# Performance work log

Hardware: AMD Instinct MI355X
Metric: run time of the kernel (lower is better)

Reference implementation:

```python
import jax, jax.numpy as jnp
import numpy as np

HIDDEN = 1024
HEADS = 16
HEAD_DIM = HIDDEN // HEADS


def setup_inputs() -> dict:
    key = jax.random.key(0)
    k0, k1, k2, k3, k4 = jax.random.split(key, 5)
    s = 0.02
    return {
        "data": jax.random.normal(k0, (4, 2048, HIDDEN), dtype=jnp.float32),
        "qkv_w": jax.random.normal(k1, (3 * HIDDEN, HIDDEN), dtype=jnp.float32) * s,  # (out,in) torch layout
        "qkv_b": jax.random.normal(k2, (3 * HIDDEN,), dtype=jnp.float32) * s,
        "out_w": jax.random.normal(k3, (HIDDEN, HIDDEN), dtype=jnp.float32) * s,
        "out_b": jax.random.normal(k4, (HIDDEN,), dtype=jnp.float32) * s,
    }


def reference(data, qkv_w, qkv_b, out_w, out_b):
    B, T, C = data.shape
    qkv = jnp.einsum("btc,oc->bto", data, qkv_w) + qkv_b  # [B,T,3C]
    q, k, v = jnp.split(qkv, 3, axis=2)
    # [B,T,C] -> [B,H,T,D]
    def heads(x):
        return x.reshape(B, T, HEADS, HEAD_DIM).transpose(0, 2, 1, 3)
    q, k, v = heads(q), heads(k), heads(v)
    scale = 1.0 / jnp.sqrt(jnp.float32(HEAD_DIM))
    att = jnp.einsum("bhqd,bhkd->bhqk", q, k) * scale  # [B,H,T,T]
    causal = jnp.tril(jnp.ones((T, T), dtype=bool))
    att = jnp.where(causal[None, None, :, :], att, -jnp.inf)
    att = jax.nn.softmax(att, axis=-1)
    out = jnp.einsum("bhqk,bhkd->bhqd", att, v)  # [B,H,T,D]
    out = out.transpose(0, 2, 1, 3).reshape(B, T, C)
    return jnp.einsum("btc,oc->bto", out, out_w) + out_b
```

## Files before the change

### kernel.cpp

```cpp
#include <hip/hip_runtime.h>
#include <hip/hip_bf16.h>
#include <stdint.h>

typedef __attribute__((ext_vector_type(8))) __bf16 bf16x8;
typedef __attribute__((ext_vector_type(4))) float f32x4;
typedef __attribute__((ext_vector_type(16))) float f32x16;
typedef __attribute__((ext_vector_type(4))) unsigned int u32x4;

#define HIDDEN 1024
#define HEADS 16
#define HD 64
#define NB 4
#define T_ 2048
#define M_ROWS (NB * T_)
#define SCL2 0.18033688f
#define FIXM 32.0f

__device__ __forceinline__ unsigned short f2bf(float x) {
  unsigned u = __builtin_bit_cast(unsigned, x);
  u += 0x7fff + ((u >> 16) & 1);
  return (unsigned short)(u >> 16);
}

__device__ __forceinline__ unsigned pk2(float a, float b) {
  unsigned ua = __builtin_bit_cast(unsigned, a) + 0x8000u;
  unsigned ub = __builtin_bit_cast(unsigned, b) + 0x8000u;
  return __builtin_amdgcn_perm(ub, ua, 0x07060302);
}

__device__ __forceinline__ f32x4 mfma16(bf16x8 a, bf16x8 b, f32x4 c) {
  return __builtin_amdgcn_mfma_f32_16x16x32_bf16(a, b, c, 0, 0, 0);
}
__device__ __forceinline__ f32x16 mfma32(bf16x8 a, bf16x8 b, f32x16 c) {
  return __builtin_amdgcn_mfma_f32_32x32x16_bf16(a, b, c, 0, 0, 0);
}

__device__ __forceinline__ void lds16(const void* g, void* l) {
  __builtin_amdgcn_global_load_lds(
      (const __attribute__((address_space(1))) unsigned int*)g,
      (__attribute__((address_space(3))) unsigned int*)l, 16, 0, 0);
}

__device__ __forceinline__ bf16x8 ldg8(const unsigned short* p) {
  return __builtin_bit_cast(bf16x8, *(const u32x4*)p);
}

__global__ void cvt_bf16(const float* __restrict__ in,
                         unsigned short* __restrict__ out, int n4) {
  int i = blockIdx.x * blockDim.x + threadIdx.x;
  int stride = gridDim.x * blockDim.x;
  for (; i < n4; i += stride) {
    float4 v = ((const float4*)in)[i];
    ushort4 o;
    o.x = f2bf(v.x); o.y = f2bf(v.y); o.z = f2bf(v.z); o.w = f2bf(v.w);
    ((ushort4*)out)[i] = o;
  }
}


#define MF4(AM, B0, B1, B2, B3, M)              \
  acc[M][0] = mfma16(AM, B0, acc[M][0]);        \
  acc[M][1] = mfma16(AM, B1, acc[M][1]);        \
  acc[M][2] = mfma16(AM, B2, acc[M][2]);        \
  acc[M][3] = mfma16(AM, B3, acc[M][3]);

#define RD(BUF, OFF) \
  __builtin_bit_cast(bf16x8, *(const u32x4*)((BUF) + (OFF)))

template <int EPI, int NT>
__global__ __launch_bounds__(512, 2) void gemm8(
    const unsigned short* __restrict__ A, const unsigned short* __restrict__ Bm,
    const float* __restrict__ bias, unsigned short* __restrict__ Qb,
    unsigned short* __restrict__ Kb, unsigned short* __restrict__ Vtb,
    float* __restrict__ Cf) {
  constexpr int K = 1024;
  constexpr int N = NT * 128;
  __shared__ __align__(16) char LB[147456];
  const int tid = threadIdx.x;
  const int wv = tid >> 6, lane = tid & 63;
  const int l16 = lane & 15, grp = lane >> 4;
  const int wm = wv >> 1, wn = wv & 1;
  const int bid = blockIdx.x;
  const int sw = (bid & 7) * (NT * 4) + (bid >> 3);
  const int by = sw / NT, bx = sw % NT;
  const int brow0 = by * 256, bcol0 = bx * 128;

  const int srow = wv * 8 + (lane >> 3);
  const int sunit = (lane & 7) ^ (srow & 7);
  const unsigned short* pA = A + (size_t)(brow0 + srow) * K + sunit * 8;
  const unsigned short* pB = Bm + (size_t)(bcol0 + srow) * K + sunit * 8;

  const int rsw = l16 & 7;
  const int swu0 = ((grp) ^ rsw) << 4;
  const int swu1 = ((4 + grp) ^ rsw) << 4;
  const int aBase = (wm * 64 + l16) * 128;
  const int bBase = (wn * 64 + l16) * 128;

#define BUFA(c) (LB + (c) * 49152)
#define BUFB(c) (LB + (c) * 49152 + 32768)
#define STAGE_A01(c, t)                                          \
  do {                                                           \
    lds16(pA + (size_t)(t) * 64, BUFA(c) + wv * 1024);           \
    lds16(pA + (size_t)64 * K + (t) * 64,                        \
          BUFA(c) + 8192 + wv * 1024);                           \
  } while (0)
#define STAGE_A23(c, t)                                          \
  do {                                                           \
    lds16(pA + (size_t)128 * K + (t) * 64,                       \
          BUFA(c) + 16384 + wv * 1024);                          \
    lds16(pA + (size_t)192 * K + (t) * 64,                       \
          BUFA(c) + 24576 + wv * 1024);                          \
  } while (0)
#define STAGE_B01(c, t)                                          \
  do {                                                           \
    lds16(pB + (size_t)(t) * 64, BUFB(c) + wv * 1024);           \
    lds16(pB + (size_t)64 * K + (t) * 64,                        \
          BUFB(c) + 8192 + wv * 1024);                           \
  } while (0)

  f32x4 acc[4][4];
#pragma unroll
  for (int m = 0; m < 4; m++)
#pragma unroll
    for (int n = 0; n < 4; n++) acc[m][n] = (f32x4){0.f, 0.f, 0.f, 0.f};

#define GTILE(BA, BB, S1, S2, S3, ENDW)                                \
  {                                                                    \
    bf16x8 b00 = RD(BB, bBase + swu0), b01 = RD(BB, bBase + 2048 + swu0), \
           b02 = RD(BB, bBase + 4096 + swu0),                          \
           b03 = RD(BB, bBase + 6144 + swu0);                          \
    bf16x8 a0 = RD(BA, aBase + swu0), a1 = RD(BA, aBase + 2048 + swu0); \
    S1;                                                                \
    __builtin_amdgcn_s_barrier();                                      \
    __builtin_amdgcn_s_setprio(1);                                     \
    MF4(a0, b00, b01, b02, b03, 0)                                     \
    MF4(a1, b00, b01, b02, b03, 1)                                     \
    __builtin_amdgcn_s_setprio(0);                                     \
    __builtin_amdgcn_s_barrier();                                      \
    bf16x8 b10 = RD(BB, bBase + swu1), b11 = RD(BB, bBase + 2048 + swu1), \
           b12 = RD(BB, bBase + 4096 + swu1),                          \
           b13 = RD(BB, bBase + 6144 + swu1);                          \
    a0 = RD(BA, aBase + swu1);                                         \
    a1 = RD(BA, aBase + 2048 + swu1);                                  \
    S2;                                                                \
    __builtin_amdgcn_s_barrier();                                      \
    __builtin_amdgcn_s_setprio(1);                                     \
    MF4(a0, b10, b11, b12, b13, 0)                                     \
    MF4(a1, b10, b11, b12, b13, 1)                                     \
    __builtin_amdgcn_s_setprio(0);                                     \
    __builtin_amdgcn_s_barrier();                                      \
    a0 = RD(BA, aBase + 4096 + swu0);                                  \
    a1 = RD(BA, aBase + 6144 + swu0);                                  \
    S3;                                                                \
    __builtin_amdgcn_s_barrier();                                      \
    __builtin_amdgcn_s_setprio(1);                                     \
    MF4(a0, b00, b01, b02, b03, 2)                                     \
    MF4(a1, b00, b01, b02, b03, 3)                                     \
    __builtin_amdgcn_s_setprio(0);                                     \
    __builtin_amdgcn_s_barrier();                                      \
    a0 = RD(BA, aBase + 4096 + swu1);                                  \
    a1 = RD(BA, aBase + 6144 + swu1);                                  \
    __builtin_amdgcn_s_barrier();                                      \
    __builtin_amdgcn_s_setprio(1);                                     \
    MF4(a0, b10, b11, b12, b13, 2)                                     \
    MF4(a1, b10, b11, b12, b13, 3)                                     \
    __builtin_amdgcn_s_setprio(0);                                     \
    ENDW;                                                              \
    __builtin_amdgcn_s_barrier();                                      \
  }

  STAGE_A01(0, 0); STAGE_A23(0, 0); STAGE_B01(0, 0);
  STAGE_A01(1, 1); STAGE_A23(1, 1); STAGE_B01(1, 1);
  asm volatile("s_waitcnt vmcnt(6)" ::: "memory");
  __builtin_amdgcn_sched_barrier(0);
  __builtin_amdgcn_s_barrier();

  int c = 0, c2 = 2;
#pragma unroll 1
  for (int t = 0; t < 14; ++t) {
    const char* ba = BUFA(c);
    const char* bb = BUFB(c);
    GTILE(ba, bb, STAGE_A01(c2, t + 2), STAGE_A23(c2, t + 2),
          STAGE_B01(c2, t + 2),
          { asm volatile("s_waitcnt vmcnt(6)" ::: "memory");
            __builtin_amdgcn_sched_barrier(0); });
    c = (c == 2) ? 0 : c + 1;
    c2 = (c2 == 2) ? 0 : c2 + 1;
  }
  {
    const char* ba = BUFA(c);
    const char* bb = BUFB(c);
    GTILE(ba, bb, , , ,
          { asm volatile("s_waitcnt vmcnt(0)" ::: "memory");
            __builtin_amdgcn_sched_barrier(0); });
    c = (c == 2) ? 0 : c + 1;
  }
  {
    const char* ba = BUFA(c);
    const char* bb = BUFB(c);
    GTILE(ba, bb, , , , );
  }

#pragma unroll
  for (int m = 0; m < 4; m++) {
#pragma unroll
    for (int n = 0; n < 4; n++) {
      int col = bcol0 + wn * 64 + n * 16 + l16;
      int row0 = brow0 + wm * 64 + m * 16 + grp * 4;
      float bs = bias[col];
      if (EPI == 0) {
        int part = col >> 10, rem = col & 1023;
        int h = rem >> 6, d = rem & 63;
#pragma unroll
        for (int r = 0; r < 4; r++) {
          int rw = row0 + r;
          int b = rw >> 11, t = rw & 2047;
          unsigned short val = f2bf(acc[m][n][r] + bs);
          size_t bh = (size_t)(b * 16 + h);
          if (part == 0)
            Qb[(bh * T_ + t) * HD + d] = val;
          else if (part == 1)
            Kb[(bh * T_ + t) * HD + d] = val;
          else {
            int k = t & 31;
            int rr = (k & 3) + 4 * (k >> 3);
            int s = (rr & 7) + 8 * ((k >> 2) & 1) + 16 * (rr >> 3);
            Vtb[(bh * HD + d) * T_ + (t & ~31) + s] = val;
          }
        }
      } else {
#pragma unroll
        for (int r = 0; r < 4; r++)
          Cf[(size_t)(row0 + r) * N + col] = acc[m][n][r] + bs;
      }
    }
  }
#undef BUFA
#undef BUFB
#undef STAGE_A01
#undef STAGE_A23
#undef STAGE_B01
#undef GTILE
}

__global__ __launch_bounds__(256, 3) void attn32(
    const unsigned short* __restrict__ Q, const unsigned short* __restrict__ K,
    const unsigned short* __restrict__ Vt, unsigned short* __restrict__ Ao) {
  __shared__ __align__(16) unsigned short Kl[2][32 * 64];
  __shared__ __align__(16) unsigned short Vl[2][32 * 64];
  const int i = blockIdx.x;
  const int bh = i & 63;
  const int g = (i < 512) ? (15 - (i >> 6)) : ((i - 512) >> 6);
  const int wv = threadIdx.x >> 6, lane = threadIdx.x & 63;
  const int l31 = lane & 31, hi = lane >> 5;
  const int qt = g * 4 + wv;
  const int maxqt = g * 4 + 3;
  const unsigned short* Qh = Q + (size_t)bh * T_ * HD;
  const unsigned short* Kh = K + (size_t)bh * T_ * HD;
  const unsigned short* Vh = Vt + (size_t)bh * HD * T_;
  const int b_ = bh >> 4, h_ = bh & 15;

  const int sj = threadIdx.x >> 3, su = threadIdx.x & 7;
  const int sup = su ^ (sj & 7);
  const unsigned short* ksrc = Kh + sj * HD + sup * 8;
  const unsigned short* vsrc =
      Vh + (size_t)(sj + 32 * (sup >> 2)) * T_ + (sup & 3) * 8;
  char* kdst0 = (char*)&Kl[0][0] + wv * 1024;
  char* kdst1 = (char*)&Kl[1][0] + wv * 1024;
  char* vdst0 = (char*)&Vl[0][0] + wv * 1024;
  char* vdst1 = (char*)&Vl[1][0] + wv * 1024;

#define STAGE(B, KC)                                     \
  do {                                                   \
    int kt_ = (KC) * 32;                                 \
    lds16(ksrc + (size_t)kt_ * HD, (B) ? kdst1 : kdst0); \
    lds16(vsrc + kt_, (B) ? vdst1 : vdst0);              \
  } while (0)

  int rdoff[4];
#pragma unroll
  for (int ks = 0; ks < 4; ks++)
    rdoff[ks] = l31 * 128 + (((2 * ks + hi) ^ (l31 & 7)) << 4);

  bf16x8 qf[4];
  const int qbase = qt * 32;
#pragma unroll
  for (int st = 0; st < 4; st++)
    qf[st] = ldg8(&Qh[(size_t)(qbase + l31) * HD + st * 16 + hi * 8]);

  f32x16 o0, o1;
#pragma unroll
  for (int r = 0; r < 16; r++) { o0[r] = 0.f; o1[r] = 0.f; }
  float rl = 0.f;

#define CHUNK(B, MASKED)                                                     \
  do {                                                                       \
    const char* kb = (const char*)&Kl[(B)][0];                               \
    const char* vb = (const char*)&Vl[(B)][0];                               \
    bf16x8 KF[4], VF[4];                                                     \
    _Pragma("unroll") for (int ks = 0; ks < 4; ks++) {                       \
      KF[ks] = __builtin_bit_cast(bf16x8, *(const u32x4*)(kb + rdoff[ks]));  \
      VF[ks] = __builtin_bit_cast(bf16x8, *(const u32x4*)(vb + rdoff[ks]));  \
    }                                                                        \
    f32x16 sa;                                                               \
    _Pragma("unroll") for (int r = 0; r < 16; r++) sa[r] = 0.f;              \
    sa = mfma32(KF[0], qf[0], sa);                                           \
    sa = mfma32(KF[1], qf[1], sa);                                           \
    sa = mfma32(KF[2], qf[2], sa);                                           \
    sa = mfma32(KF[3], qf[3], sa);                                           \
    float pv[16];                                                            \
    _Pragma("unroll") for (int r = 0; r < 16; r++) {                         \
      float arg = __builtin_fmaf(sa[r], SCL2, -FIXM);                        \
      if (MASKED) {                                                          \
        int key = (r & 3) + 8 * (r >> 2) + 4 * hi;                           \
        if (key > l31) arg = -1e30f;                                         \
      }                                                                      \
      pv[r] = exp2f(arg);                                                    \
      rl += pv[r];                                                           \
    }                                                                        \
    u32x4 pa0u, pa1u;                                                        \
    pa0u.x = pk2(pv[0], pv[1]);                                              \
    pa0u.y = pk2(pv[2], pv[3]);                                              \
    pa0u.z = pk2(pv[4], pv[5]);                                              \
    pa0u.w = pk2(pv[6], pv[7]);                                              \
    pa1u.x = pk2(pv[8], pv[9]);                                              \
    pa1u.y = pk2(pv[10], pv[11]);                                            \
    pa1u.z = pk2(pv[12], pv[13]);                                            \
    pa1u.w = pk2(pv[14], pv[15]);                                            \
    bf16x8 pa0 = __builtin_bit_cast(bf16x8, pa0u);                           \
    bf16x8 pa1 = __builtin_bit_cast(bf16x8, pa1u);                           \
    o0 = mfma32(VF[0], pa0, o0);                                             \
    o0 = mfma32(VF[1], pa1, o0);                                             \
    o1 = mfma32(VF[2], pa0, o1);                                             \
    o1 = mfma32(VF[3], pa1, o1);                                             \
  } while (0)

  STAGE(0, 0);
  __syncthreads();
  int cur = 0;
  for (int kc = 0; kc <= maxqt; kc++) {
    if (kc < maxqt) STAGE(cur ^ 1, kc + 1);
    if (kc < qt) {
      CHUNK(cur, 0);
    } else if (kc == qt) {
      CHUNK(cur, 1);
    }
    __syncthreads();
    cur ^= 1;
  }

  float rlt = rl + __shfl_xor(rl, 32);
  float inv = 1.f / rlt;
  const size_t base =
      ((size_t)b_ * T_ + qbase + l31) * HIDDEN + h_ * HD + hi * 4;
#pragma unroll
  for (int gg = 0; gg < 4; gg++) {
    uint2 u;
    u.x = pk2(o0[4 * gg] * inv, o0[4 * gg + 1] * inv);
    u.y = pk2(o0[4 * gg + 2] * inv, o0[4 * gg + 3] * inv);
    *(uint2*)&Ao[base + gg * 8] = u;
  }
#pragma unroll
  for (int gg = 0; gg < 4; gg++) {
    uint2 u;
    u.x = pk2(o1[4 * gg] * inv, o1[4 * gg + 1] * inv);
    u.y = pk2(o1[4 * gg + 2] * inv, o1[4 * gg + 3] * inv);
    *(uint2*)&Ao[base + 32 + gg * 8] = u;
  }
#undef STAGE
#undef CHUNK
}

extern "C" void kernel_launch(void* const* d_in, const int* in_sizes, int n_in,
                              void* d_out, int out_size, void* d_ws,
                              size_t ws_size, hipStream_t stream) {
  const float* data = (const float*)d_in[0];
  const float* qkvw = (const float*)d_in[1];
  const float* qkvb = (const float*)d_in[2];
  const float* outw = (const float*)d_in[3];
  const float* outb = (const float*)d_in[4];
  float* out = (float*)d_out;
  char* ws = (char*)d_ws;

  unsigned short* dataBf = (unsigned short*)(ws);
  unsigned short* qkvwBf = (unsigned short*)(ws + 16777216);
  unsigned short* outwBf = (unsigned short*)(ws + 23068672);
  unsigned short* Qb = (unsigned short*)(ws + 25165824);
  unsigned short* Kb = (unsigned short*)(ws + 41943040);
  unsigned short* Vtb = (unsigned short*)(ws + 58720256);
  unsigned short* attnO = dataBf;

  cvt_bf16<<<2048, 256, 0, stream>>>(data, dataBf, (M_ROWS * HIDDEN) / 4);
  cvt_bf16<<<1024, 256, 0, stream>>>(qkvw, qkvwBf, (3 * HIDDEN * HIDDEN) / 4);
  cvt_bf16<<<512, 256, 0, stream>>>(outw, outwBf, (HIDDEN * HIDDEN) / 4);

  gemm8<0, 24><<<768, 512, 0, stream>>>(dataBf, qkvwBf, qkvb, Qb, Kb, Vtb,
                                        nullptr);
  attn32<<<1024, 256, 0, stream>>>(Qb, Kb, Vtb, attnO);
  gemm8<1, 8><<<256, 512, 0, stream>>>(attnO, outwBf, outb, nullptr, nullptr,
                                       nullptr, out);
}
```

Baseline: 188.1 us.

## Stage 64-key tiles per barrier in attention and fuse bf16 conversion kernels

The attention kernel now stages 64 keys of K and V per double-buffered stage, in two 32-row halves, instead of 32. Each barrier then covers two 32-key chunks, halving the number of __syncthreads and stage issues per block, at the cost of twice the LDS per buffer. The causal diagonal chunk is handled by processing half 0 unmasked and half 1 masked when the query tile index is odd, or only half 0 masked when it is even. Separately, the three fp32-to-bf16 conversion launches are merged into a single grid-stride kernel with a per-element branch, removing two launches.

```diff
diff --git a/kernel.cpp b/kernel.cpp
--- a/kernel.cpp
+++ b/kernel.cpp
@@ -45,15 +45,29 @@
   return __builtin_bit_cast(bf16x8, *(const u32x4*)p);
 }
 
-__global__ void cvt_bf16(const float* __restrict__ in,
-                         unsigned short* __restrict__ out, int n4) {
+__global__ void cvt3(const float* __restrict__ i0, unsigned short* __restrict__ o0,
+                     int n0, const float* __restrict__ i1,
+                     unsigned short* __restrict__ o1, int n1,
+                     const float* __restrict__ i2,
+                     unsigned short* __restrict__ o2, int n2) {
   int i = blockIdx.x * blockDim.x + threadIdx.x;
   int stride = gridDim.x * blockDim.x;
-  for (; i < n4; i += stride) {
-    float4 v = ((const float4*)in)[i];
+  int tot = n0 + n1 + n2;
+  for (; i < tot; i += stride) {
+    const float* src;
+    unsigned short* dst;
+    int j = i;
+    if (j < n0) {
+      src = i0; dst = o0;
+    } else if ((j -= n0) < n1) {
+      src = i1; dst = o1;
+    } else {
+      j -= n1; src = i2; dst = o2;
+    }
+    float4 v = ((const float4*)src)[j];
     ushort4 o;
     o.x = f2bf(v.x); o.y = f2bf(v.y); o.z = f2bf(v.z); o.w = f2bf(v.w);
-    ((ushort4*)out)[i] = o;
+    ((ushort4*)dst)[j] = o;
   }
 }
 
@@ -98,24 +112,24 @@
 
 #define BUFA(c) (LB + (c) * 49152)
 #define BUFB(c) (LB + (c) * 49152 + 32768)
-#define STAGE_A01(c, t)                                          \
-  do {                                                           \
-    lds16(pA + (size_t)(t) * 64, BUFA(c) + wv * 1024);           \
-    lds16(pA + (size_t)64 * K + (t) * 64,                        \
-          BUFA(c) + 8192 + wv * 1024);                           \
+#define STAGE_A01(c, t)                                \
+  do {                                                 \
+    lds16(pA + (size_t)(t) * 64, BUFA(c) + wv * 1024); \
+    lds16(pA + (size_t)64 * K + (t) * 64,              \
+          BUFA(c) + 8192 + wv * 1024);                 \
   } while (0)
-#define STAGE_A23(c, t)                                          \
-  do {                                                           \
-    lds16(pA + (size_t)128 * K + (t) * 64,                       \
-          BUFA(c) + 16384 + wv * 1024);                          \
-    lds16(pA + (size_t)192 * K + (t) * 64,                       \
-          BUFA(c) + 24576 + wv * 1024);                          \
+#define STAGE_A23(c, t)                                \
+  do {                                                 \
+    lds16(pA + (size_t)128 * K + (t) * 64,             \
+          BUFA(c) + 16384 + wv * 1024);                \
+    lds16(pA + (size_t)192 * K + (t) * 64,             \
+          BUFA(c) + 24576 + wv * 1024);                \
   } while (0)
-#define STAGE_B01(c, t)                                          \
-  do {                                                           \
-    lds16(pB + (size_t)(t) * 64, BUFB(c) + wv * 1024);           \
-    lds16(pB + (size_t)64 * K + (t) * 64,                        \
-          BUFB(c) + 8192 + wv * 1024);                           \
+#define STAGE_B01(c, t)                                \
+  do {                                                 \
+    lds16(pB + (size_t)(t) * 64, BUFB(c) + wv * 1024); \
+    lds16(pB + (size_t)64 * K + (t) * 64,              \
+          BUFB(c) + 8192 + wv * 1024);                 \
   } while (0)
 
   f32x4 acc[4][4];
@@ -124,49 +138,49 @@
 #pragma unroll
     for (int n = 0; n < 4; n++) acc[m][n] = (f32x4){0.f, 0.f, 0.f, 0.f};
 
-#define GTILE(BA, BB, S1, S2, S3, ENDW)                                \
-  {                                                                    \
+#define GTILE(BA, BB, S1, S2, S3, ENDW)                                   \
+  {                                                                       \
     bf16x8 b00 = RD(BB, bBase + swu0), b01 = RD(BB, bBase + 2048 + swu0), \
-           b02 = RD(BB, bBase + 4096 + swu0),                          \
-           b03 = RD(BB, bBase + 6144 + swu0);                          \
-    bf16x8 a0 = RD(BA, aBase + swu0), a1 = RD(BA, aBase + 2048 + swu0); \
-    S1;                                                                \
-    __builtin_amdgcn_s_barrier();                                      \
-    __builtin_amdgcn_s_setprio(1);                                     \
-    MF4(a0, b00, b01, b02, b03, 0)                                     \
-    MF4(a1, b00, b01, b02, b03, 1)                                     \
-    __builtin_amdgcn_s_setprio(0);                                     \
-    __builtin_amdgcn_s_barrier();                                      \
+           b02 = RD(BB, bBase + 4096 + swu0),                             \
+           b03 = RD(BB, bBase + 6144 + swu0);                             \
+    bf16x8 a0 = RD(BA, aBase + swu0), a1 = RD(BA, aBase + 2048 + swu0);   \
+    S1;                                                                   \
+    __builtin_amdgcn_s_barrier();                                         \
+    __builtin_amdgcn_s_setprio(1);                                        \
+    MF4(a0, b00, b01, b02, b03, 0)                                        \
+    MF4(a1, b00, b01, b02, b03, 1)                                        \
+    __builtin_amdgcn_s_setprio(0);                                        \
+    __builtin_amdgcn_s_barrier();                                         \
     bf16x8 b10 = RD(BB, bBase + swu1), b11 = RD(BB, bBase + 2048 + swu1), \
-           b12 = RD(BB, bBase + 4096 + swu1),                          \
-           b13 = RD(BB, bBase + 6144 + swu1);                          \
-    a0 = RD(BA, aBase + swu1);                                         \
-    a1 = RD(BA, aBase + 2048 + swu1);                                  \
-    S2;                                                                \
-    __builtin_amdgcn_s_barrier();                                      \
-    __builtin_amdgcn_s_setprio(1);                                     \
-    MF4(a0, b10, b11, b12, b13, 0)                                     \
-    MF4(a1, b10, b11, b12, b13, 1)                                     \
-    __builtin_amdgcn_s_setprio(0);                                     \
-    __builtin_amdgcn_s_barrier();                                      \
-    a0 = RD(BA, aBase + 4096 + swu0);                                  \
-    a1 = RD(BA, aBase + 6144 + swu0);                                  \
-    S3;                                                                \
-    __builtin_amdgcn_s_barrier();                                      \
-    __builtin_amdgcn_s_setprio(1);                                     \
-    MF4(a0, b00, b01, b02, b03, 2)                                     \
-    MF4(a1, b00, b01, b02, b03, 3)                                     \
-    __builtin_amdgcn_s_setprio(0);                                     \
-    __builtin_amdgcn_s_barrier();                                      \
-    a0 = RD(BA, aBase + 4096 + swu1);                                  \
-    a1 = RD(BA, aBase + 6144 + swu1);                                  \
-    __builtin_amdgcn_s_barrier();                                      \
-    __builtin_amdgcn_s_setprio(1);                                     \
-    MF4(a0, b10, b11, b12, b13, 2)                                     \
-    MF4(a1, b10, b11, b12, b13, 3)                                     \
-    __builtin_amdgcn_s_setprio(0);                                     \
-    ENDW;                                                              \
-    __builtin_amdgcn_s_barrier();                                      \
+           b12 = RD(BB, bBase + 4096 + swu1),                             \
+           b13 = RD(BB, bBase + 6144 + swu1);                             \
+    a0 = RD(BA, aBase + swu1);                                            \
+    a1 = RD(BA, aBase + 2048 + swu1);                                     \
+    S2;                                                                   \
+    __builtin_amdgcn_s_barrier();                                         \
+    __builtin_amdgcn_s_setprio(1);                                        \
+    MF4(a0, b10, b11, b12, b13, 0)                                        \
+    MF4(a1, b10, b11, b12, b13, 1)                                        \
+    __builtin_amdgcn_s_setprio(0);                                        \
+    __builtin_amdgcn_s_barrier();                                         \
+    a0 = RD(BA, aBase + 4096 + swu0);                                     \
+    a1 = RD(BA, aBase + 6144 + swu0);                                     \
+    S3;                                                                   \
+    __builtin_amdgcn_s_barrier();                                         \
+    __builtin_amdgcn_s_setprio(1);                                        \
+    MF4(a0, b00, b01, b02, b03, 2)                                        \
+    MF4(a1, b00, b01, b02, b03, 3)                                        \
+    __builtin_amdgcn_s_setprio(0);                                        \
+    __builtin_amdgcn_s_barrier();                                         \
+    a0 = RD(BA, aBase + 4096 + swu1);                                     \
+    a1 = RD(BA, aBase + 6144 + swu1);                                     \
+    __builtin_amdgcn_s_barrier();                                         \
+    __builtin_amdgcn_s_setprio(1);                                        \
+    MF4(a0, b10, b11, b12, b13, 2)                                        \
+    MF4(a1, b10, b11, b12, b13, 3)                                        \
+    __builtin_amdgcn_s_setprio(0);                                        \
+    ENDW;                                                                 \
+    __builtin_amdgcn_s_barrier();                                         \
   }
 
   STAGE_A01(0, 0); STAGE_A23(0, 0); STAGE_B01(0, 0);
@@ -243,18 +257,19 @@
 #undef GTILE
 }
 
+
 __global__ __launch_bounds__(256, 3) void attn32(
     const unsigned short* __restrict__ Q, const unsigned short* __restrict__ K,
     const unsigned short* __restrict__ Vt, unsigned short* __restrict__ Ao) {
-  __shared__ __align__(16) unsigned short Kl[2][32 * 64];
-  __shared__ __align__(16) unsigned short Vl[2][32 * 64];
+  __shared__ __align__(16) unsigned short Kl[2][64 * 64];
+  __shared__ __align__(16) unsigned short Vl[2][64 * 64];
   const int i = blockIdx.x;
   const int bh = i & 63;
   const int g = (i < 512) ? (15 - (i >> 6)) : ((i - 512) >> 6);
   const int wv = threadIdx.x >> 6, lane = threadIdx.x & 63;
   const int l31 = lane & 31, hi = lane >> 5;
   const int qt = g * 4 + wv;
-  const int maxqt = g * 4 + 3;
+  const int kmax = g * 2 + 1;
   const unsigned short* Qh = Q + (size_t)bh * T_ * HD;
   const unsigned short* Kh = K + (size_t)bh * T_ * HD;
   const unsigned short* Vh = Vt + (size_t)bh * HD * T_;
@@ -265,16 +280,16 @@
   const unsigned short* ksrc = Kh + sj * HD + sup * 8;
   const unsigned short* vsrc =
       Vh + (size_t)(sj + 32 * (sup >> 2)) * T_ + (sup & 3) * 8;
-  char* kdst0 = (char*)&Kl[0][0] + wv * 1024;
-  char* kdst1 = (char*)&Kl[1][0] + wv * 1024;
-  char* vdst0 = (char*)&Vl[0][0] + wv * 1024;
-  char* vdst1 = (char*)&Vl[1][0] + wv * 1024;
-
-#define STAGE(B, KC)                                     \
-  do {                                                   \
-    int kt_ = (KC) * 32;                                 \
-    lds16(ksrc + (size_t)kt_ * HD, (B) ? kdst1 : kdst0); \
-    lds16(vsrc + kt_, (B) ? vdst1 : vdst0);              \
+
+#define STAGE(B, C2)                                                      \
+  do {                                                                    \
+    int kt_ = (C2) * 64;                                                  \
+    char* kd = (char*)&Kl[(B)][0] + wv * 1024;                            \
+    char* vd = (char*)&Vl[(B)][0] + wv * 1024;                            \
+    lds16(ksrc + (size_t)kt_ * HD, kd);                                   \
+    lds16(ksrc + (size_t)(kt_ + 32) * HD, kd + 4096);                     \
+    lds16(vsrc + kt_, vd);                                                \
+    lds16(vsrc + kt_ + 32, vd + 4096);                                    \
   } while (0)
 
   int rdoff[4];
@@ -293,10 +308,10 @@
   for (int r = 0; r < 16; r++) { o0[r] = 0.f; o1[r] = 0.f; }
   float rl = 0.f;
 
-#define CHUNK(B, MASKED)                                                     \
+#define CHUNKH(B, H, MASKED)                                                 \
   do {                                                                       \
-    const char* kb = (const char*)&Kl[(B)][0];                               \
-    const char* vb = (const char*)&Vl[(B)][0];                               \
+    const char* kb = (const char*)&Kl[(B)][0] + (H) * 4096;                  \
+    const char* vb = (const char*)&Vl[(B)][0] + (H) * 4096;                  \
     bf16x8 KF[4], VF[4];                                                     \
     _Pragma("unroll") for (int ks = 0; ks < 4; ks++) {                       \
       KF[ks] = __builtin_bit_cast(bf16x8, *(const u32x4*)(kb + rdoff[ks]));  \
@@ -338,12 +353,19 @@
   STAGE(0, 0);
   __syncthreads();
   int cur = 0;
-  for (int kc = 0; kc <= maxqt; kc++) {
-    if (kc < maxqt) STAGE(cur ^ 1, kc + 1);
-    if (kc < qt) {
-      CHUNK(cur, 0);
-    } else if (kc == qt) {
-      CHUNK(cur, 1);
+  const int halfq = qt >> 1, oddq = qt & 1;
+  for (int kc2 = 0; kc2 <= kmax; kc2++) {
+    if (kc2 < kmax) STAGE(cur ^ 1, kc2 + 1);
+    if (kc2 < halfq) {
+      CHUNKH(cur, 0, 0);
+      CHUNKH(cur, 1, 0);
+    } else if (kc2 == halfq) {
+      if (oddq) {
+        CHUNKH(cur, 0, 0);
+        CHUNKH(cur, 1, 1);
+      } else {
+        CHUNKH(cur, 0, 1);
+      }
     }
     __syncthreads();
     cur ^= 1;
@@ -368,7 +390,7 @@
     *(uint2*)&Ao[base + 32 + gg * 8] = u;
   }
 #undef STAGE
-#undef CHUNK
+#undef CHUNKH
 }
 
 extern "C" void kernel_launch(void* const* d_in, const int* in_sizes, int n_in,
@@ -390,9 +412,9 @@
   unsigned short* Vtb = (unsigned short*)(ws + 58720256);
   unsigned short* attnO = dataBf;
 
-  cvt_bf16<<<2048, 256, 0, stream>>>(data, dataBf, (M_ROWS * HIDDEN) / 4);
-  cvt_bf16<<<1024, 256, 0, stream>>>(qkvw, qkvwBf, (3 * HIDDEN * HIDDEN) / 4);
-  cvt_bf16<<<512, 256, 0, stream>>>(outw, outwBf, (HIDDEN * HIDDEN) / 4);
+  cvt3<<<2048, 256, 0, stream>>>(data, dataBf, (M_ROWS * HIDDEN) / 4, qkvw,
+                                 qkvwBf, (3 * HIDDEN * HIDDEN) / 4, outw,
+                                 outwBf, (HIDDEN * HIDDEN) / 4);
 
   gemm8<0, 24><<<768, 512, 0, stream>>>(dataBf, qkvwBf, qkvb, Qb, Kb, Vtb,
                                         nullptr);
```

After: 187.5 us. About the same (-0.3%).
